# Kernel tuning notes

Hardware: AMD Instinct MI355X
Metric: run time of the kernel (lower is better)

The kernel has to match this reference:

```python
import jax, jax.numpy as jnp
import numpy as np
import math

N = 4096      # n_history
D = 512       # embed_dim
H = 8         # time-weight MLP hidden size


def setup_inputs() -> dict:
    key = jax.random.key(0)
    k1, k2, k3, k4, k5 = jax.random.split(key, 5)
    return {
        "query_code_embeds": jax.random.normal(k1, (N, D), dtype=jnp.float32),
        "hist_embeddings": jax.random.normal(k2, (N, D), dtype=jnp.float32),
        "hist_times": jax.random.uniform(k3, (N,), dtype=jnp.float32),
        "tw_w1": jax.random.normal(k4, (1, H), dtype=jnp.float32) * (1.0 / math.sqrt(1.0)),
        "tw_b1": jnp.zeros((H,), dtype=jnp.float32),
        "tw_w2": jax.random.normal(k5, (H, 1), dtype=jnp.float32) * (1.0 / math.sqrt(H)),
        "tw_b2": jnp.zeros((1,), dtype=jnp.float32),
    }


def reference(query_code_embeds, hist_embeddings, hist_times, tw_w1, tw_b1, tw_w2, tw_b2):
    # pairwise absolute time differences: [n, n, 1]
    time_diffs = jnp.abs(hist_times[:, None] - hist_times[None, :])[..., None]
    # pointwise MLP on time diffs -> multiplicative attention bias [n, n]
    h = jax.nn.relu(time_diffs @ tw_w1 + tw_b1)            # [n, n, H]
    time_weights = jax.nn.sigmoid(h @ tw_w2 + tw_b2)[..., 0]  # [n, n]
    # scaled dot-product scores modulated by time weights
    scores = (query_code_embeds @ hist_embeddings.T) / math.sqrt(D)
    scores = scores * time_weights
    attn = jax.nn.softmax(scores, axis=1)
    return attn @ hist_embeddings
```

## Files before the change

kernel.cpp:

```cpp
#include <hip/hip_runtime.h>

#define N 4096
#define D 512
#define FRAG_SH 512
#define NTHR 256
#define SC_STRIDE 136
#define SMEM_BYTES 69632

typedef __attribute__((ext_vector_type(8))) short short8;
typedef __attribute__((ext_vector_type(4))) float f32x4;

__device__ __forceinline__ unsigned short f2bf(float f) {
    unsigned int u = __float_as_uint(f);
    u = (u + 0x7FFFu + ((u >> 16) & 1u)) >> 16;
    return (unsigned short)u;
}
__device__ __forceinline__ unsigned short f2bf_rn(float f) {
    return (unsigned short)((__float_as_uint(f) + 0x8000u) >> 16);
}
__device__ __forceinline__ float bf2f(unsigned short u) {
    return __uint_as_float((unsigned)u << 16);
}

__global__ __launch_bounds__(NTHR) void prep_kernel(
    const float* __restrict__ q, const float* __restrict__ hist,
    unsigned short* __restrict__ Qblk, unsigned short* __restrict__ Kblk,
    unsigned short* __restrict__ Vblk, float* __restrict__ dsum)
{
    __shared__ unsigned short smem[32 * 512];
    const int bid = blockIdx.x, tid = threadIdx.x;
    if (bid >= 256) {
        int z = (bid - 256) * NTHR + tid;
        #pragma unroll
        for (int j = 0; j < 8; ++j) dsum[z * 8 + j] = 0.f;
        return;
    }
    const bool isQ = bid < 128;
    const int t = isQ ? bid : bid - 128;
    const float* src = isQ ? q : hist;
    const float scale = isQ ? 0.04419417382415922f : 1.0f;

    #pragma unroll
    for (int k = 0; k < 16; ++k) {
        int idx = tid + k * 256;
        int row = idx >> 7;
        int c4  = (idx & 127) << 2;
        float4 v = *(const float4*)(src + (size_t)(t * 32 + row) * D + c4);
        ushort4 o;
        o.x = f2bf(v.x * scale); o.y = f2bf(v.y * scale);
        o.z = f2bf(v.z * scale); o.w = f2bf(v.w * scale);
        *(ushort4*)(smem + row * 512 + c4) = o;
    }
    __syncthreads();

    unsigned short* ABdst = isQ ? Qblk : Kblk;
    #pragma unroll
    for (int k = 0; k < 8; ++k) {
        int s = tid + k * 256;
        int fl = s >> 6, ln = s & 63;
        int dk = fl >> 1, rbl = fl & 1;
        int l16 = ln & 15, qq = ln >> 4;
        short8 v = *(const short8*)(smem + (rbl * 16 + l16) * 512 + dk * 32 + qq * 8);
        *(short8*)(ABdst + ((size_t)dk * 256 + t * 2 + rbl) * FRAG_SH + ln * 8) = v;
    }
    if (!isQ) {
        #pragma unroll
        for (int k = 0; k < 8; ++k) {
            int s = tid + k * 256;
            int db = s >> 6, ln = s & 63;
            int l16 = ln & 15, qq = ln >> 4;
            unsigned short tmp[8];
            #pragma unroll
            for (int j = 0; j < 8; ++j)
                tmp[j] = smem[(qq * 8 + j) * 512 + db * 16 + l16];
            *(short8*)(Vblk + ((size_t)t * 32 + db) * FRAG_SH + ln * 8) = *(const short8*)tmp;
        }
    }
}

__global__ __launch_bounds__(NTHR, 2) void qk_kernel(
    const unsigned short* __restrict__ Qblk, const unsigned short* __restrict__ Kblk,
    const float* __restrict__ times,
    const float* __restrict__ w1, const float* __restrict__ b1,
    const float* __restrict__ w2, const float* __restrict__ b2,
    unsigned short* __restrict__ Pblk, float* __restrict__ dsum)
{
    extern __shared__ unsigned short smem[];
    const int tid = threadIdx.x, bid = blockIdx.x;
    const int wv = tid >> 6, lane = tid & 63;
    const int qq = lane >> 4, l16 = lane & 15;
    const int wy = wv >> 1, wx = wv & 1;
    const int cg = ((bid & 7) << 1) | ((bid >> 3) & 1);
    const int rg = bid >> 4;

    f32x4 acc[4][8];
    #pragma unroll
    for (int fy = 0; fy < 4; ++fy)
        #pragma unroll
        for (int fx = 0; fx < 8; ++fx) acc[fy][fx] = (f32x4){0.f, 0.f, 0.f, 0.f};

    for (int dk = 0; dk < 16; ++dk) {
        short8 a[4], b[8];
        #pragma unroll
        for (int fy = 0; fy < 4; ++fy)
            a[fy] = *(const short8*)(Qblk + ((size_t)dk * 256 + rg * 8 + wy * 4 + fy) * FRAG_SH + lane * 8);
        #pragma unroll
        for (int fx = 0; fx < 8; ++fx)
            b[fx] = *(const short8*)(Kblk + ((size_t)dk * 256 + cg * 16 + wx * 8 + fx) * FRAG_SH + lane * 8);
        #pragma unroll
        for (int fy = 0; fy < 4; ++fy)
            #pragma unroll
            for (int fx = 0; fx < 8; ++fx)
                acc[fy][fx] = __builtin_amdgcn_mfma_f32_16x16x32_bf16(a[fy], b[fx], acc[fy][fx], 0, 0, 0);
    }

    float w1v[8], b1v[8], w2v[8];
    #pragma unroll
    for (int k = 0; k < 8; ++k) { w1v[k] = w1[k]; b1v[k] = b1[k]; w2v[k] = w2[k]; }
    const float b2v = b2[0];
    bool fast = true;
    #pragma unroll
    for (int k = 0; k < 8; ++k) fast = fast && (b1v[k] == 0.0f);
    float C1 = 0.0f;
    #pragma unroll
    for (int k = 0; k < 8; ++k) C1 += w2v[k] * fmaxf(w1v[k], 0.0f);

    const int rowbase = rg * 128 + wy * 64;
    const int colbase = cg * 256 + wx * 128;
    float tcol[8];
    #pragma unroll
    for (int fx = 0; fx < 8; ++fx) tcol[fx] = times[colbase + fx * 16 + l16];

    unsigned short* sc = smem + wv * (64 * SC_STRIDE);
    #pragma unroll
    for (int fy = 0; fy < 4; ++fy) {
        #pragma unroll
        for (int ri = 0; ri < 4; ++ri) {
            const float tq = times[rowbase + fy * 16 + qq * 4 + ri];
            float se = 0.f;
            #pragma unroll
            for (int fx = 0; fx < 8; ++fx) {
                float td = fabsf(tq - tcol[fx]);
                float a = fmaf(td, C1, b2v);
                if (!fast) {
                    a = b2v;
                    #pragma unroll
                    for (int k = 0; k < 8; ++k)
                        a += w2v[k] * fmaxf(fmaf(td, w1v[k], b1v[k]), 0.f);
                }
                float twt = __builtin_amdgcn_rcpf(1.0f + __expf(-a));
                float e = __expf(acc[fy][fx][ri] * twt);
                se += e;
                sc[(fy * 16 + qq * 4 + ri) * SC_STRIDE + fx * 16 + l16] = f2bf_rn(e);
            }
            se += __shfl_xor(se, 1);
            se += __shfl_xor(se, 2);
            se += __shfl_xor(se, 4);
            se += __shfl_xor(se, 8);
            if (l16 == 0) atomicAdd(dsum + rowbase + fy * 16 + qq * 4 + ri, se);
        }
    }
    #pragma unroll
    for (int fy = 0; fy < 4; ++fy)
        #pragma unroll
        for (int kb = 0; kb < 4; ++kb) {
            short8 v = *(const short8*)(sc + (fy * 16 + l16) * SC_STRIDE + kb * 32 + qq * 8);
            size_t fidx = (size_t)(cg * 8 + wx * 4 + kb) * 256 + (rg * 8 + wy * 4 + fy);
            *(short8*)(Pblk + fidx * FRAG_SH + lane * 8) = v;
        }
}

__global__ __launch_bounds__(NTHR, 2) void pv_kernel(
    const unsigned short* __restrict__ Pblk, const unsigned short* __restrict__ Vblk,
    unsigned short* __restrict__ Opart, int iters)
{
    const int tid = threadIdx.x;
    const int wv = tid >> 6, lane = tid & 63;
    const int qq = lane >> 4, l16 = lane & 15;
    const int chunk = blockIdx.x;
    const int rg = blockIdx.y;
    const int kbase = chunk * iters;

    f32x4 acc[2][8];
    #pragma unroll
    for (int fy = 0; fy < 2; ++fy)
        #pragma unroll
        for (int fx = 0; fx < 8; ++fx) acc[fy][fx] = (f32x4){0.f, 0.f, 0.f, 0.f};

    for (int it = 0; it < iters; ++it) {
        const int kb32 = kbase + it;
        short8 a[2], b[8];
        #pragma unroll
        for (int fy = 0; fy < 2; ++fy)
            a[fy] = *(const short8*)(Pblk + ((size_t)kb32 * 256 + rg * 2 + fy) * FRAG_SH + lane * 8);
        #pragma unroll
        for (int fx = 0; fx < 8; ++fx)
            b[fx] = *(const short8*)(Vblk + ((size_t)kb32 * 32 + wv * 8 + fx) * FRAG_SH + lane * 8);
        #pragma unroll
        for (int fy = 0; fy < 2; ++fy)
            #pragma unroll
            for (int fx = 0; fx < 8; ++fx)
                acc[fy][fx] = __builtin_amdgcn_mfma_f32_16x16x32_bf16(a[fy], b[fx], acc[fy][fx], 0, 0, 0);
    }

    unsigned short* ob = Opart + (size_t)chunk * N * D;
    #pragma unroll
    for (int fy = 0; fy < 2; ++fy)
        #pragma unroll
        for (int ri = 0; ri < 4; ++ri) {
            const int row = rg * 32 + fy * 16 + qq * 4 + ri;
            #pragma unroll
            for (int fx = 0; fx < 8; ++fx) {
                const int col = wv * 128 + fx * 16 + l16;
                ob[(size_t)row * D + col] = f2bf_rn(acc[fy][fx][ri]);
            }
        }
}

__global__ __launch_bounds__(NTHR) void reduce_kernel(
    const unsigned short* __restrict__ Opart, const float* __restrict__ dsum,
    float* __restrict__ out, int KS2)
{
    int i = blockIdx.x * NTHR + threadIdx.x;
    int row = i >> 7;
    float inv = 1.0f / dsum[row];
    float4 acc = {0.f, 0.f, 0.f, 0.f};
    for (int c = 0; c < KS2; ++c) {
        ushort4 u = ((const ushort4*)(Opart + (size_t)c * N * D))[i];
        acc.x += bf2f(u.x); acc.y += bf2f(u.y);
        acc.z += bf2f(u.z); acc.w += bf2f(u.w);
    }
    acc.x *= inv; acc.y *= inv; acc.z *= inv; acc.w *= inv;
    ((float4*)out)[i] = acc;
}

extern "C" void kernel_launch(void* const* d_in, const int* in_sizes, int n_in,
                              void* d_out, int out_size, void* d_ws, size_t ws_size,
                              hipStream_t stream) {
    const float* q     = (const float*)d_in[0];
    const float* hist  = (const float*)d_in[1];
    const float* times = (const float*)d_in[2];
    const float* w1    = (const float*)d_in[3];
    const float* b1    = (const float*)d_in[4];
    const float* w2    = (const float*)d_in[5];
    const float* b2    = (const float*)d_in[6];
    float* out = (float*)d_out;

    char* base = (char*)d_ws;
    const size_t MB4 = (size_t)N * D * 2;
    unsigned short* Vblk = (unsigned short*)base;
    unsigned short* Pblk = (unsigned short*)(base + MB4);
    float* dsum          = (float*)(base + MB4 + (size_t)N * (size_t)N * 2);
    char* ob             = base + MB4 + (size_t)N * (size_t)N * 2 + 65536;
    unsigned short* Qblk = (unsigned short*)ob;
    unsigned short* Kblk = (unsigned short*)(ob + MB4);
    unsigned short* Opart = (unsigned short*)ob;
    const size_t fixed = (size_t)(ob - base);
    const int KS2 = (ws_size >= fixed + 8 * MB4) ? 8 :
                    (ws_size >= fixed + 4 * MB4) ? 4 : 2;
    const int iters = (N / 32) / KS2;

    hipFuncSetAttribute((const void*)qk_kernel,
                        hipFuncAttributeMaxDynamicSharedMemorySize, SMEM_BYTES);

    prep_kernel<<<258, NTHR, 0, stream>>>(q, hist, Qblk, Kblk, Vblk, dsum);
    qk_kernel<<<512, NTHR, SMEM_BYTES, stream>>>(Qblk, Kblk, times, w1, b1, w2, b2, Pblk, dsum);
    pv_kernel<<<dim3(KS2, 128), NTHR, 0, stream>>>(Pblk, Vblk, Opart, iters);
    reduce_kernel<<<(N * D / 4) / NTHR, NTHR, 0, stream>>>(Opart, dsum, out, KS2);
}
```

Before: 150.1 us.

## Halve QK tile width, double-buffer fragment loads, cap PV split-K at four

The QK kernel's per-block column tile shrinks from 256 to 128, giving 1024 blocks, halving accumulator registers and switching to static shared memory. Both the QK and PV kernels now double-buffer their global fragment loads so the next k-step's loads are issued before the current MFMAs run. The PV split-K factor is capped at 4 instead of 8, which cuts partial-output traffic in the reduce at the cost of fewer PV blocks. Smaller QK tiles reuse each loaded fragment less and issue twice as many dsum atomics, while the prefetch buffers add register pressure.

```diff
diff --git a/kernel.cpp b/kernel.cpp
--- a/kernel.cpp
+++ b/kernel.cpp
@@ -4,8 +4,8 @@
 #define D 512
 #define FRAG_SH 512
 #define NTHR 256
-#define SC_STRIDE 136
-#define SMEM_BYTES 69632
+#define SC_STRIDE 68
+#define SMEM_BYTES 34816
 
 typedef __attribute__((ext_vector_type(8))) short short8;
 typedef __attribute__((ext_vector_type(4))) float f32x4;
@@ -85,34 +85,44 @@
     const float* __restrict__ w2, const float* __restrict__ b2,
     unsigned short* __restrict__ Pblk, float* __restrict__ dsum)
 {
-    extern __shared__ unsigned short smem[];
+    __shared__ unsigned short smem[4 * 64 * SC_STRIDE];
     const int tid = threadIdx.x, bid = blockIdx.x;
     const int wv = tid >> 6, lane = tid & 63;
     const int qq = lane >> 4, l16 = lane & 15;
     const int wy = wv >> 1, wx = wv & 1;
-    const int cg = ((bid & 7) << 1) | ((bid >> 3) & 1);
-    const int rg = bid >> 4;
-
-    f32x4 acc[4][8];
+    const int cg = ((bid & 7) << 2) | ((bid >> 3) & 3);
+    const int rg = bid >> 5;
+
+    f32x4 acc[4][4];
     #pragma unroll
     for (int fy = 0; fy < 4; ++fy)
         #pragma unroll
-        for (int fx = 0; fx < 8; ++fx) acc[fy][fx] = (f32x4){0.f, 0.f, 0.f, 0.f};
-
+        for (int fx = 0; fx < 4; ++fx) acc[fy][fx] = (f32x4){0.f, 0.f, 0.f, 0.f};
+
+    short8 abuf[2][4], bbuf[2][4];
+    #define LOADAB(dk, s)                                                              \
+        {                                                                              \
+            _Pragma("unroll")                                                          \
+            for (int fy = 0; fy < 4; ++fy)                                             \
+                abuf[s][fy] = *(const short8*)(Qblk + ((size_t)(dk) * 256 + rg * 8 + wy * 4 + fy) * FRAG_SH + lane * 8); \
+            _Pragma("unroll")                                                          \
+            for (int fx = 0; fx < 4; ++fx)                                             \
+                bbuf[s][fx] = *(const short8*)(Kblk + ((size_t)(dk) * 256 + cg * 8 + wx * 4 + fx) * FRAG_SH + lane * 8); \
+        }
+
+    LOADAB(0, 0);
+    #pragma unroll
     for (int dk = 0; dk < 16; ++dk) {
-        short8 a[4], b[8];
+        const int cur = dk & 1;
+        if (dk < 15) LOADAB(dk + 1, cur ^ 1);
         #pragma unroll
         for (int fy = 0; fy < 4; ++fy)
-            a[fy] = *(const short8*)(Qblk + ((size_t)dk * 256 + rg * 8 + wy * 4 + fy) * FRAG_SH + lane * 8);
-        #pragma unroll
-        for (int fx = 0; fx < 8; ++fx)
-            b[fx] = *(const short8*)(Kblk + ((size_t)dk * 256 + cg * 16 + wx * 8 + fx) * FRAG_SH + lane * 8);
-        #pragma unroll
-        for (int fy = 0; fy < 4; ++fy)
-            #pragma unroll
-            for (int fx = 0; fx < 8; ++fx)
-                acc[fy][fx] = __builtin_amdgcn_mfma_f32_16x16x32_bf16(a[fy], b[fx], acc[fy][fx], 0, 0, 0);
-    }
+            #pragma unroll
+            for (int fx = 0; fx < 4; ++fx)
+                acc[fy][fx] = __builtin_amdgcn_mfma_f32_16x16x32_bf16(
+                    abuf[cur][fy], bbuf[cur][fx], acc[fy][fx], 0, 0, 0);
+    }
+    #undef LOADAB
 
     float w1v[8], b1v[8], w2v[8];
     #pragma unroll
@@ -126,10 +136,10 @@
     for (int k = 0; k < 8; ++k) C1 += w2v[k] * fmaxf(w1v[k], 0.0f);
 
     const int rowbase = rg * 128 + wy * 64;
-    const int colbase = cg * 256 + wx * 128;
-    float tcol[8];
-    #pragma unroll
-    for (int fx = 0; fx < 8; ++fx) tcol[fx] = times[colbase + fx * 16 + l16];
+    const int colbase = cg * 128 + wx * 64;
+    float tcol[4];
+    #pragma unroll
+    for (int fx = 0; fx < 4; ++fx) tcol[fx] = times[colbase + fx * 16 + l16];
 
     unsigned short* sc = smem + wv * (64 * SC_STRIDE);
     #pragma unroll
@@ -139,7 +149,7 @@
             const float tq = times[rowbase + fy * 16 + qq * 4 + ri];
             float se = 0.f;
             #pragma unroll
-            for (int fx = 0; fx < 8; ++fx) {
+            for (int fx = 0; fx < 4; ++fx) {
                 float td = fabsf(tq - tcol[fx]);
                 float a = fmaf(td, C1, b2v);
                 if (!fast) {
@@ -163,9 +173,9 @@
     #pragma unroll
     for (int fy = 0; fy < 4; ++fy)
         #pragma unroll
-        for (int kb = 0; kb < 4; ++kb) {
+        for (int kb = 0; kb < 2; ++kb) {
             short8 v = *(const short8*)(sc + (fy * 16 + l16) * SC_STRIDE + kb * 32 + qq * 8);
-            size_t fidx = (size_t)(cg * 8 + wx * 4 + kb) * 256 + (rg * 8 + wy * 4 + fy);
+            size_t fidx = (size_t)(cg * 4 + wx * 2 + kb) * 256 + (rg * 8 + wy * 4 + fy);
             *(short8*)(Pblk + fidx * FRAG_SH + lane * 8) = v;
         }
 }
@@ -187,21 +197,29 @@
         #pragma unroll
         for (int fx = 0; fx < 8; ++fx) acc[fy][fx] = (f32x4){0.f, 0.f, 0.f, 0.f};
 
+    short8 abuf[2][2], bbuf[2][8];
+    #define LOADPV(kb32, s)                                                            \
+        {                                                                              \
+            _Pragma("unroll")                                                          \
+            for (int fy = 0; fy < 2; ++fy)                                             \
+                abuf[s][fy] = *(const short8*)(Pblk + ((size_t)(kb32) * 256 + rg * 2 + fy) * FRAG_SH + lane * 8); \
+            _Pragma("unroll")                                                          \
+            for (int fx = 0; fx < 8; ++fx)                                             \
+                bbuf[s][fx] = *(const short8*)(Vblk + ((size_t)(kb32) * 32 + wv * 8 + fx) * FRAG_SH + lane * 8); \
+        }
+
+    LOADPV(kbase, 0);
     for (int it = 0; it < iters; ++it) {
-        const int kb32 = kbase + it;
-        short8 a[2], b[8];
+        const int cur = it & 1;
+        if (it + 1 < iters) LOADPV(kbase + it + 1, cur ^ 1);
         #pragma unroll
         for (int fy = 0; fy < 2; ++fy)
-            a[fy] = *(const short8*)(Pblk + ((size_t)kb32 * 256 + rg * 2 + fy) * FRAG_SH + lane * 8);
-        #pragma unroll
-        for (int fx = 0; fx < 8; ++fx)
-            b[fx] = *(const short8*)(Vblk + ((size_t)kb32 * 32 + wv * 8 + fx) * FRAG_SH + lane * 8);
-        #pragma unroll
-        for (int fy = 0; fy < 2; ++fy)
             #pragma unroll
             for (int fx = 0; fx < 8; ++fx)
-                acc[fy][fx] = __builtin_amdgcn_mfma_f32_16x16x32_bf16(a[fy], b[fx], acc[fy][fx], 0, 0, 0);
-    }
+                acc[fy][fx] = __builtin_amdgcn_mfma_f32_16x16x32_bf16(
+                    abuf[cur][fy], bbuf[cur][fx], acc[fy][fx], 0, 0, 0);
+    }
+    #undef LOADPV
 
     unsigned short* ob = Opart + (size_t)chunk * N * D;
     #pragma unroll
@@ -256,15 +274,11 @@
     unsigned short* Kblk = (unsigned short*)(ob + MB4);
     unsigned short* Opart = (unsigned short*)ob;
     const size_t fixed = (size_t)(ob - base);
-    const int KS2 = (ws_size >= fixed + 8 * MB4) ? 8 :
-                    (ws_size >= fixed + 4 * MB4) ? 4 : 2;
+    const int KS2 = (ws_size >= fixed + 4 * MB4) ? 4 : 2;
     const int iters = (N / 32) / KS2;
 
-    hipFuncSetAttribute((const void*)qk_kernel,
-                        hipFuncAttributeMaxDynamicSharedMemorySize, SMEM_BYTES);
-
     prep_kernel<<<258, NTHR, 0, stream>>>(q, hist, Qblk, Kblk, Vblk, dsum);
-    qk_kernel<<<512, NTHR, SMEM_BYTES, stream>>>(Qblk, Kblk, times, w1, b1, w2, b2, Pblk, dsum);
+    qk_kernel<<<1024, NTHR, 0, stream>>>(Qblk, Kblk, times, w1, b1, w2, b2, Pblk, dsum);
     pv_kernel<<<dim3(KS2, 128), NTHR, 0, stream>>>(Pblk, Vblk, Opart, iters);
     reduce_kernel<<<(N * D / 4) / NTHR, NTHR, 0, stream>>>(Opart, dsum, out, KS2);
 }
```

Result: slower. 480.5 us (+220.1%).
